# Optimization experiments

Hardware: AMD Instinct MI355X
Metric: run time of the kernel (lower is better)

## Reference

```python
import jax, jax.numpy as jnp
import numpy as np


def _norm(H, add):
    # Faithful port of GTN.norm: transpose, zero diagonal (optionally add self-loop),
    # row-degree inverse scaling, transpose back.
    Ht = H.T
    n = Ht.shape[0]
    eye = jnp.eye(n, dtype=H.dtype)
    Ht = Ht * (1.0 - eye) + (eye if add else 0.0)
    deg = jnp.sum(Ht, axis=1)
    dinv = jnp.where(deg == 0, 0.0, 1.0 / deg)
    return (dinv[:, None] * Ht).T


def _lstm(x, h0, c0, wih, whh, bih, bhh):
    # x: [B, S, D]; single-layer batch_first LSTM, PyTorch gate order (i, f, g, o).
    def step(carry, xt):
        h, c = carry
        gates = xt @ wih.T + h @ whh.T + bih + bhh
        i, f, g, o = jnp.split(gates, 4, axis=-1)
        i = jax.nn.sigmoid(i); f = jax.nn.sigmoid(f)
        g = jnp.tanh(g); o = jax.nn.sigmoid(o)
        c = f * c + i * g
        h = o * jnp.tanh(c)
        return (h, c), h
    (_, _), ys = jax.lax.scan(step, (h0, c0), jnp.transpose(x, (1, 0, 2)))
    return jnp.transpose(ys, (1, 0, 2))  # [B, S, U]


def _forward(A, X, seq_len, seqs, h0, c0, w1a, w1b, w2,
             gcn_w, lin1_w, lin1_b, lstm_wih, lstm_whh, lstm_bih, lstm_bhh, out_w):
    N = A.shape[0]
    B, S, _ = seqs.shape
    A4 = jnp.transpose(A, (2, 0, 1))  # [E, N, N]

    def gtconv(w):  # w: [C, E], softmax over edge-type channels
        return jnp.einsum('enm,ce->cnm', A4, jax.nn.softmax(w, axis=1))

    # layer 0 (first=True): H = conv1(A) @ conv2(A)
    H = jnp.matmul(gtconv(w1a), gtconv(w1b))  # [C, N, N]
    # layer 1: normalize per channel, then H = H_ @ conv1(A)
    Hn = jax.vmap(lambda h: _norm(h, False))(H)
    H = jnp.matmul(Hn, gtconv(w2))

    # gcn_conv per channel: relu(norm(H_c, add=True).T @ (X @ W)), concat over channels
    Hg = jax.vmap(lambda h: _norm(h, True))(H)  # [C, N, N]
    Xw = X @ gcn_w                              # [N, w_out]
    Xc = jax.nn.relu(jnp.einsum('cnm,nw->cmw', Hg, Xw))  # [C, N, w_out]
    X_ = jnp.transpose(Xc, (1, 0, 2)).reshape(N, -1) @ lin1_w.T + lin1_b  # [N, w_out]

    # ragged basket max-pool: masked segment-max over multi-hot baskets
    mask = seqs != 0                                           # [B, S, I]
    pooled = jnp.max(jnp.where(mask[:, :, :, None], X_[None, None], -jnp.inf), axis=2)
    basket_seqs = jnp.where(mask.any(axis=2)[..., None], pooled, 0.0)  # [B, S, w_out]

    lstm_out = _lstm(basket_seqs, h0[0], c0[0], lstm_wih, lstm_whh, lstm_bih, lstm_bhh)
    idx = jnp.clip(seq_len - 1, 0, S - 1)
    actual = lstm_out[jnp.arange(B), idx]      # [B, U]
    return jax.nn.sigmoid(actual @ out_w.T)    # [B, nb_items]


def setup_inputs() -> dict:
    N, E, C, WIN, WOUT, B, S, U = 2048, 4, 2, 64, 64, 16, 20, 256
    I = N  # nb_items
    key = jax.random.key(0)
    ks = jax.random.split(key, 16)
    A = jax.random.uniform(ks[0], (N, N, E), dtype=jnp.float32)
    X = jax.random.normal(ks[1], (N, WIN), dtype=jnp.float32)
    seq_len = jax.random.randint(ks[2], (B,), 1, S + 1)
    # sparse multi-hot baskets (~20 items per basket)
    seqs = (jax.random.uniform(ks[3], (B, S, I)) < 0.01).astype(jnp.int32)
    h0 = jnp.zeros((1, B, U), dtype=jnp.float32)
    c0 = jnp.zeros((1, B, U), dtype=jnp.float32)
    w1a = 0.1 * jax.random.normal(ks[4], (C, E), dtype=jnp.float32)
    w1b = 0.1 * jax.random.normal(ks[5], (C, E), dtype=jnp.float32)
    w2 = 0.1 * jax.random.normal(ks[6], (C, E), dtype=jnp.float32)
    gcn_w = jax.random.normal(ks[7], (WIN, WOUT), dtype=jnp.float32) / np.sqrt(WIN)
    lin1_w = 0.05 * jax.random.normal(ks[8], (WOUT, C * WOUT), dtype=jnp.float32)
    lin1_b = jnp.zeros((WOUT,), dtype=jnp.float32)
    lstm_wih = 0.05 * jax.random.normal(ks[9], (4 * U, WOUT), dtype=jnp.float32)
    lstm_whh = 0.05 * jax.random.normal(ks[10], (4 * U, U), dtype=jnp.float32)
    lstm_bih = jnp.zeros((4 * U,), dtype=jnp.float32)
    lstm_bhh = jnp.zeros((4 * U,), dtype=jnp.float32)
    out_w = 0.05 * jax.random.normal(ks[11], (I, U), dtype=jnp.float32)
    return {"A": A, "X": X, "seq_len": seq_len, "seqs": seqs, "h0": h0, "c0": c0,
            "w1a": w1a, "w1b": w1b, "w2": w2, "gcn_w": gcn_w,
            "lin1_w": lin1_w, "lin1_b": lin1_b, "lstm_wih": lstm_wih,
            "lstm_whh": lstm_whh, "lstm_bih": lstm_bih, "lstm_bhh": lstm_bhh,
            "out_w": out_w}


def reference(A, X, seq_len, seqs, h0, c0, w1a, w1b, w2, gcn_w, lin1_w, lin1_b,
              lstm_wih, lstm_whh, lstm_bih, lstm_bhh, out_w):
    return _forward(A, X, seq_len, seqs, h0, c0, w1a, w1b, w2, gcn_w,
                    lin1_w, lin1_b, lstm_wih, lstm_whh, lstm_bih, lstm_bhh, out_w)
```

## Files before the change

### kernel.cpp

```cpp
#include <hip/hip_runtime.h>
#include <hip/hip_fp16.h>
#include <math.h>

#define NN_ 2048
#define EE_ 4
#define CC_ 2
#define BB_ 16
#define SS_ 20
#define UU_ 256

#define LREGB 80
#define LLDSB 48

typedef __attribute__((ext_vector_type(8))) short short8;
typedef __attribute__((ext_vector_type(4))) float f32x4;
typedef _Float16 half2v __attribute__((ext_vector_type(2)));

__device__ __forceinline__ unsigned short f2bf(float x){
    union { float f; unsigned int u; } v; v.f = x;
    unsigned int u = v.u;
    unsigned int r = u + 0x7FFFu + ((u >> 16) & 1u);
    return (unsigned short)(r >> 16);
}
__device__ __forceinline__ float bf2f(unsigned short s){
    union { unsigned int u; float f; } v; v.u = ((unsigned int)s) << 16; return v.f;
}

__device__ __forceinline__ half2v u2h2(unsigned int u){
    union { unsigned int u; half2v h; } c; c.u = u; return c.h;
}

__device__ __forceinline__ float dot2f(unsigned int w, unsigned int h, float acc){
#if __has_builtin(__builtin_amdgcn_fdot2)
    return __builtin_amdgcn_fdot2(u2h2(w), u2h2(h), acc, false);
#else
    float w0 = __half2float(__ushort_as_half((unsigned short)(w & 0xffffu)));
    float w1 = __half2float(__ushort_as_half((unsigned short)(w >> 16)));
    float h0f = __half2float(__ushort_as_half((unsigned short)(h & 0xffffu)));
    float h1f = __half2float(__ushort_as_half((unsigned short)(h >> 16)));
    return fmaf(w1, h1f, fmaf(w0, h0f, acc));
#endif
}

__device__ __forceinline__ float sigf(float x){
    x = fminf(fmaxf(x, -30.f), 30.f);
    float e = __builtin_amdgcn_exp2f(-1.442695041f * x);
    return __builtin_amdgcn_rcpf(1.f + e);
}
__device__ __forceinline__ float tanhf_(float x){
    x = fminf(fmaxf(x, -15.f), 15.f);
    float e = __builtin_amdgcn_exp2f(2.885390082f * x);
    return (e - 1.f) * __builtin_amdgcn_rcpf(e + 1.f);
}

typedef const __attribute__((address_space(1))) unsigned int* gas_ptr;
typedef __attribute__((address_space(3))) unsigned int* las_ptr;
__device__ __forceinline__ void gl_lds16(const void* g, void* l){
    __builtin_amdgcn_global_load_lds((gas_ptr)g, (las_ptr)l, 16, 0, 0);
}

__global__ void k_softmax(const float* __restrict__ w1a, const float* __restrict__ w1b,
                          const float* __restrict__ w2, float* __restrict__ sm){
    int t = threadIdx.x;
    if (t < 6){
        int widx = t >> 1, c = t & 1;
        const float* w = (widx==0)? w1a : ((widx==1)? w1b : w2);
        float v[EE_]; float m = -1e30f;
        for (int e=0;e<EE_;e++){ v[e]=w[c*EE_+e]; m=fmaxf(m,v[e]); }
        float s=0.f;
        for (int e=0;e<EE_;e++){ v[e]=expf(v[e]-m); s+=v[e]; }
        for (int e=0;e<EE_;e++) sm[widx*8 + c*4 + e] = v[e]/s;
    }
}

__global__ __launch_bounds__(256) void k_conv_bf16(const float4* __restrict__ A4,
        const float* __restrict__ sm, unsigned short* __restrict__ convA,
        unsigned short* __restrict__ convBT, unsigned short* __restrict__ convCT){
    __shared__ float4 tile[32][33];
    int bx = blockIdx.x*32, by = blockIdx.y*32;
    int tx = threadIdx.x & 31, ty = threadIdx.x >> 5;
    #pragma unroll
    for (int i=0;i<32;i+=8){
        int n = by+ty+i, m = bx+tx;
        float4 a = A4[(size_t)n*NN_ + m];
        tile[ty+i][tx] = a;
        #pragma unroll
        for (int cc=0;cc<CC_;cc++){
            const float* s = sm + cc*4;
            convA[(size_t)cc*NN_*NN_ + (size_t)n*NN_ + m] =
                f2bf(a.x*s[0]+a.y*s[1]+a.z*s[2]+a.w*s[3]);
        }
    }
    __syncthreads();
    #pragma unroll
    for (int i=0;i<32;i+=8){
        int x = bx+ty+i, y = by+tx;
        float4 a = tile[tx][ty+i];
        #pragma unroll
        for (int cc=0;cc<CC_;cc++){
            const float* s1 = sm + 8 + cc*4;
            const float* s2 = sm + 16 + cc*4;
            convBT[(size_t)cc*NN_*NN_ + (size_t)x*NN_ + y] =
                f2bf(a.x*s1[0]+a.y*s1[1]+a.z*s1[2]+a.w*s1[3]);
            convCT[(size_t)cc*NN_*NN_ + (size_t)x*NN_ + y] =
                f2bf(a.x*s2[0]+a.y*s2[1]+a.z*s2[2]+a.w*s2[3]);
        }
    }
}

__global__ __launch_bounds__(256) void k_mfma_gemm(const unsigned short* __restrict__ Abase,
        const unsigned short* __restrict__ Bbase, unsigned short* __restrict__ Cbase,
        float* __restrict__ colbase){
    const int c = blockIdx.z;
    const unsigned short* Ag = Abase + (size_t)c*NN_*NN_;
    const unsigned short* Bg = Bbase + (size_t)c*NN_*NN_;
    unsigned short* Cg = Cbase + (size_t)c*NN_*NN_;
    float* colacc = colbase + c*NN_;

    __shared__ __align__(16) unsigned short As[128*32];
    __shared__ __align__(16) unsigned short Bs[128*32];

    const int t = threadIdx.x;
    const int wave = t >> 6, lane = t & 63;
    const int m0 = blockIdx.y*128, n0 = blockIdx.x*128;
    const int wm = wave >> 1, wn = wave & 1;

    f32x4 acc[4][4];
    const f32x4 z = {0.f,0.f,0.f,0.f};
    #pragma unroll
    for (int i=0;i<4;i++)
        #pragma unroll
        for (int j=0;j<4;j++) acc[i][j] = z;

    const int srow = wave*32 + (lane>>2);
    const int scol = (lane&3)*8;
    const unsigned short* agp0 = Ag + (size_t)(m0+srow)*NN_ + scol;
    const unsigned short* agp1 = agp0 + (size_t)16*NN_;
    const unsigned short* bgp0 = Bg + (size_t)(n0+srow)*NN_ + scol;
    const unsigned short* bgp1 = bgp0 + (size_t)16*NN_;
    unsigned short* alp0 = &As[wave*1024];
    unsigned short* alp1 = &As[wave*1024 + 512];
    unsigned short* blp0 = &Bs[wave*1024];
    unsigned short* blp1 = &Bs[wave*1024 + 512];

    const int fr = lane & 15;
    const int fk = (lane >> 4) * 8;

    for (int k0=0; k0<NN_; k0+=32){
        gl_lds16(agp0, alp0);
        gl_lds16(agp1, alp1);
        gl_lds16(bgp0, blp0);
        gl_lds16(bgp1, blp1);
        agp0 += 32; agp1 += 32; bgp0 += 32; bgp1 += 32;
        __syncthreads();
        short8 af[4], bf[4];
        #pragma unroll
        for (int i=0;i<4;i++){
            af[i] = *(const short8*)&As[(wm*64 + i*16 + fr)*32 + fk];
            bf[i] = *(const short8*)&Bs[(wn*64 + i*16 + fr)*32 + fk];
        }
        #pragma unroll
        for (int i=0;i<4;i++)
            #pragma unroll
            for (int j=0;j<4;j++)
                acc[i][j] = __builtin_amdgcn_mfma_f32_16x16x32_bf16(af[i], bf[j], acc[i][j], 0, 0, 0);
        __syncthreads();
    }

    #pragma unroll
    for (int j=0;j<4;j++){
        int col = n0 + wn*64 + j*16 + (lane & 15);
        float cs = 0.f;
        #pragma unroll
        for (int i=0;i<4;i++){
            int row = m0 + wm*64 + i*16 + (lane>>4)*4;
            #pragma unroll
            for (int r=0;r<4;r++){
                Cg[(size_t)(row+r)*NN_ + col] = f2bf(acc[i][j][r]);
                cs += acc[i][j][r];
            }
        }
        atomicAdd(&colacc[col], cs);
    }
}

template<bool ADD>
__global__ void k_dinv(float* acc, const unsigned short* __restrict__ H){
    int id = blockIdx.x*256 + threadIdx.x;
    int c = id / NN_, m = id % NN_;
    float diag = bf2f(H[(size_t)c*NN_*NN_ + (size_t)m*NN_ + m]);
    float s = acc[id] - diag + (ADD ? 1.f : 0.f);
    acc[id] = (s==0.f) ? 0.f : 1.f/s;
}

__global__ __launch_bounds__(256) void k_hn(const unsigned short* __restrict__ H1,
        const float* __restrict__ dinv, unsigned short* __restrict__ Hn){
    int id = blockIdx.x*256 + threadIdx.x;
    int c = id >> 20;
    int rem = id & ((NN_*NN_/4)-1);
    int m = rem >> 9;
    int k4 = (rem & (NN_/4 - 1)) * 4;
    ushort4 h = *(const ushort4*)&H1[(size_t)c*NN_*NN_ + (size_t)m*NN_ + k4];
    float4 d = *(const float4*)&dinv[c*NN_ + k4];
    ushort4 o;
    o.x = f2bf((m==k4  ) ? 0.f : bf2f(h.x)*d.x);
    o.y = f2bf((m==k4+1) ? 0.f : bf2f(h.y)*d.y);
    o.z = f2bf((m==k4+2) ? 0.f : bf2f(h.z)*d.z);
    o.w = f2bf((m==k4+3) ? 0.f : bf2f(h.w)*d.w);
    *(ushort4*)&Hn[(size_t)c*NN_*NN_ + (size_t)m*NN_ + k4] = o;
}

__global__ __launch_bounds__(256) void k_xw(const float* __restrict__ X, const float* __restrict__ W,
                                            float* __restrict__ Xw){
    __shared__ float Ws[64*64];
    int t = threadIdx.x;
    for (int i=t;i<4096;i+=256) Ws[i]=W[i];
    __syncthreads();
    int id = blockIdx.x*256 + t;
    int n = id >> 6, w = id & 63;
    float s = 0.f;
    #pragma unroll 8
    for (int j=0;j<64;j++) s = fmaf(X[n*64+j], Ws[j*64+w], s);
    Xw[id] = s;
}

__global__ __launch_bounds__(256) void k_gcn(const unsigned short* __restrict__ H2,
                                             const float* __restrict__ Xw, float* __restrict__ Y){
    int c = blockIdx.z;
    int m0 = blockIdx.y*64;
    int n0 = blockIdx.x*256;
    const unsigned short* Hc = H2 + (size_t)c*NN_*NN_;
    __shared__ float Hs[16][68];
    __shared__ float Xs[16][68];
    int t = threadIdx.x;
    int tm = t>>4, tn = t&15;
    float acc[4][4] = {};
    for (int nb=n0; nb<n0+256; nb+=16){
        int row = t>>4, c4 = (t&15)<<2;
        ushort4 h4 = *(const ushort4*)&Hc[(size_t)(nb+row)*NN_ + m0 + c4];
        Hs[row][c4+0]=bf2f(h4.x); Hs[row][c4+1]=bf2f(h4.y);
        Hs[row][c4+2]=bf2f(h4.z); Hs[row][c4+3]=bf2f(h4.w);
        *(float4*)&Xs[row][c4] = *(const float4*)&Xw[(nb+row)*64 + c4];
        __syncthreads();
        #pragma unroll
        for (int k=0;k<16;k++){
            float4 av = *(const float4*)&Hs[k][tm*4];
            float4 bv = *(const float4*)&Xs[k][tn*4];
            float a[4] = {av.x,av.y,av.z,av.w};
            float b[4] = {bv.x,bv.y,bv.z,bv.w};
            #pragma unroll
            for (int i=0;i<4;i++)
                #pragma unroll
                for (int j=0;j<4;j++)
                    acc[i][j] = fmaf(a[i], b[j], acc[i][j]);
        }
        __syncthreads();
    }
    #pragma unroll
    for (int i=0;i<4;i++)
        #pragma unroll
        for (int j=0;j<4;j++)
            atomicAdd(&Y[((size_t)c*NN_ + m0+tm*4+i)*64 + tn*4+j], acc[i][j]);
}

__global__ void k_gcn_epi(const float* __restrict__ Y, const unsigned short* __restrict__ H2,
                          const float* __restrict__ Xw, const float* __restrict__ dinv2,
                          float* __restrict__ Xcat){
    int id = blockIdx.x*256 + threadIdx.x;
    int c = id >> 17;
    int rem = id & 131071;
    int m = rem >> 6, w = rem & 63;
    float diag = bf2f(H2[(size_t)c*NN_*NN_ + (size_t)m*NN_ + m]);
    float xwv = Xw[m*64+w];
    float v = dinv2[c*NN_+m] * (Y[id] - diag*xwv + xwv);
    Xcat[m*128 + c*64 + w] = fmaxf(v, 0.f);
}

__global__ __launch_bounds__(256) void k_lin1(const float* __restrict__ Xcat, const float* __restrict__ W,
                                              const float* __restrict__ b, float* __restrict__ Xf){
    __shared__ float WT[128*64];
    __shared__ float bs[64];
    int t = threadIdx.x;
    for (int i=t;i<8192;i+=256){ int o = i>>7, j = i&127; WT[j*64+o] = W[i]; }
    if (t<64) bs[t]=b[t];
    __syncthreads();
    int id = blockIdx.x*256 + t;
    int m = id>>6, o = id&63;
    float s = bs[o];
    #pragma unroll 8
    for (int j=0;j<128;j++) s = fmaf(Xcat[m*128+j], WT[j*64+o], s);
    Xf[id] = s;
}

__global__ __launch_bounds__(256) void k_pool(const int* __restrict__ seqs, const float* __restrict__ Xf,
                                              float* __restrict__ bask){
    int bs_id = blockIdx.x;
    __shared__ int idxbuf[NN_];
    __shared__ int cnt;
    __shared__ float red[4][64];
    int t = threadIdx.x;
    if (t==0) cnt=0;
    __syncthreads();
    const int* row = seqs + (size_t)bs_id*NN_;
    for (int i=t;i<NN_;i+=256){
        if (row[i] != 0){ int p = atomicAdd(&cnt,1); idxbuf[p]=i; }
    }
    __syncthreads();
    int nc = cnt;
    int g = t>>6, w = t&63;
    float mx = -INFINITY;
    for (int p=g;p<nc;p+=4) mx = fmaxf(mx, Xf[idxbuf[p]*64 + w]);
    red[g][w]=mx;
    __syncthreads();
    if (t<64){
        float m = fmaxf(fmaxf(red[0][t],red[1][t]),fmaxf(red[2][t],red[3][t]));
        bask[bs_id*64+t] = (nc>0)? m : 0.f;
    }
}

__global__ void k_transpose(const float* __restrict__ src, float* __restrict__ dst, int R, int Cc){
    __shared__ float tile[32][33];
    int bx = blockIdx.x*32, by = blockIdx.y*32;
    int tx = threadIdx.x, ty = threadIdx.y;
    #pragma unroll
    for (int i=0;i<32;i+=8) tile[ty+i][tx] = src[(size_t)(by+ty+i)*Cc + bx+tx];
    __syncthreads();
    #pragma unroll
    for (int i=0;i<32;i+=8) dst[(size_t)(bx+ty+i)*R + by+tx] = tile[tx][ty+i];
}

__global__ __launch_bounds__(256) void k_packw2(const float* __restrict__ whh, unsigned int* __restrict__ W2k){
    int id = blockIdx.x*256 + threadIdx.x;
    int rem = id >> 7;
    int jp  = id & 127;
    float2 v = *(const float2*)&whh[(size_t)rem*256 + 2*jp];
    unsigned int lo = __half_as_ushort(__float2half(v.x));
    unsigned int hi = __half_as_ushort(__float2half(v.y));
    W2k[id] = lo | (hi << 16);
}

__global__ __launch_bounds__(256) void k_gih(const float* __restrict__ bask, const float* __restrict__ wihT,
                                             const float* __restrict__ bih, const float* __restrict__ bhh,
                                             float* __restrict__ G){
    int id = blockIdx.x*256 + threadIdx.x;
    int r = id >> 10, o = id & 1023;
    float s = bih[o] + bhh[o];
    #pragma unroll 8
    for (int j=0;j<64;j++) s = fmaf(bask[r*64+j], wihT[j*1024+o], s);
    G[id] = s;
}

__global__ __launch_bounds__(512, 2) void k_lstm4(const unsigned int* __restrict__ W2k,
        const float* __restrict__ G, const float* __restrict__ h0, const float* __restrict__ c0,
        const int* __restrict__ seqlen, float* __restrict__ actual){
    const int b = blockIdx.x;
    const int t = threadIdx.x;
    const int u = t & 255;
    const int half_ = t >> 8;
    const int g0 = 2*half_;
    const int g1 = g0 + 1;

    __shared__ unsigned int Wl[LLDSB][2][256];
    __shared__ unsigned int hpk[128];
    __shared__ float xg[256], xo[256];

    for (int k=0;k<LLDSB;k++){
        int idx = k*512 + t;
        int jj = idx >> 9, rem = idx & 511;
        int hf = rem >> 8, uu = rem & 255;
        ((unsigned int*)Wl)[idx] = W2k[(size_t)((2*hf+1)*256 + uu)*128 + LREGB + jj];
    }
    unsigned int wA[128], wB[LREGB];
    const unsigned int* pA = W2k + (size_t)(g0*256 + u)*128;
    const unsigned int* pB = W2k + (size_t)(g1*256 + u)*128;
    #pragma unroll
    for (int jp=0;jp<128;jp++) wA[jp] = pA[jp];
    #pragma unroll
    for (int jp=0;jp<LREGB;jp++) wB[jp] = pB[jp];

    float cv = 0.f;
    if (half_==0){
        cv = c0[b*256+u];
        ((__half*)hpk)[u] = __float2half(h0[b*256+u]);
    }
    int sl = seqlen[b]-1;
    int idx_b = sl<0?0:(sl>SS_-1?SS_-1:sl);
    __syncthreads();

    const float* gbase = G + (size_t)b*SS_*1024;
    for (int s=0;s<SS_;s++){
        float gA = gbase[s*1024 + g0*256 + u];
        float gB = gbase[s*1024 + g1*256 + u];
        float aA[4] = {0.f,0.f,0.f,0.f};
        float aB[4] = {0.f,0.f,0.f,0.f};
        #pragma unroll
        for (int jp=0;jp<LREGB;jp++){
            unsigned int hp = hpk[jp];
            aA[jp&3] = dot2f(wA[jp], hp, aA[jp&3]);
            aB[jp&3] = dot2f(wB[jp], hp, aB[jp&3]);
        }
        #pragma unroll
        for (int jp=LREGB;jp<128;jp++){
            unsigned int hp = hpk[jp];
            aA[jp&3] = dot2f(wA[jp], hp, aA[jp&3]);
            aB[jp&3] = dot2f(Wl[jp-LREGB][half_][u], hp, aB[jp&3]);
        }
        float accA = (aA[0]+aA[1]) + (aA[2]+aA[3]) + gA;
        float accB = (aB[0]+aB[1]) + (aB[2]+aB[3]) + gB;
        float iv = 0.f, fv = 0.f;
        if (half_){
            xg[u] = tanhf_(accA);
            xo[u] = sigf(accB);
        } else {
            iv = sigf(accA);
            fv = sigf(accB);
        }
        __syncthreads();
        if (!half_){
            cv = fv*cv + iv*xg[u];
            float hv = xo[u]*tanhf_(cv);
            if (s==idx_b) actual[b*256+u] = hv;
            ((__half*)hpk)[u] = __float2half(hv);
        }
        __syncthreads();
    }
}

__global__ __launch_bounds__(256) void k_final(const float* __restrict__ actual, const float* __restrict__ owT,
                                               float* __restrict__ out){
    __shared__ float as_[256];
    int t = threadIdx.x;
    int b = blockIdx.x >> 3;
    int i0 = (blockIdx.x & 7) * 256;
    as_[t] = actual[b*256+t];
    __syncthreads();
    int i = i0 + t;
    float s = 0.f;
    #pragma unroll 8
    for (int u=0;u<256;u++) s = fmaf(as_[u], owT[u*2048 + i], s);
    out[b*2048 + i] = 1.f/(1.f+expf(-s));
}

extern "C" void kernel_launch(void* const* d_in, const int* in_sizes, int n_in,
                              void* d_out, int out_size, void* d_ws, size_t ws_size,
                              hipStream_t stream){
    const float* A     = (const float*)d_in[0];
    const float* X     = (const float*)d_in[1];
    const int*   seqln = (const int*)  d_in[2];
    const int*   seqs  = (const int*)  d_in[3];
    const float* h0    = (const float*)d_in[4];
    const float* c0    = (const float*)d_in[5];
    const float* w1a   = (const float*)d_in[6];
    const float* w1b   = (const float*)d_in[7];
    const float* w2    = (const float*)d_in[8];
    const float* gcn_w = (const float*)d_in[9];
    const float* lin1w = (const float*)d_in[10];
    const float* lin1b = (const float*)d_in[11];
    const float* wih   = (const float*)d_in[12];
    const float* whh   = (const float*)d_in[13];
    const float* bih   = (const float*)d_in[14];
    const float* bhh   = (const float*)d_in[15];
    const float* out_w = (const float*)d_in[16];
    float* out = (float*)d_out;

    char* ws = (char*)d_ws;
    size_t off = 0;
    auto alloc = [&](size_t bytes)->char*{
        char* p = ws + off; off += (bytes + 255) & ~(size_t)255; return p;
    };
    float* sm     = (float*)alloc(24*4);
    float* dinv1  = (float*)alloc(CC_*NN_*4);
    float* dinv2  = (float*)alloc(CC_*NN_*4);
    float* Xw     = (float*)alloc((size_t)NN_*64*4);
    float* Xcat   = (float*)alloc((size_t)NN_*128*4);
    float* Xf     = (float*)alloc((size_t)NN_*64*4);
    float* Ybuf   = (float*)alloc((size_t)CC_*NN_*64*4);
    float* bask   = (float*)alloc((size_t)BB_*SS_*64*4);
    float* Gih    = (float*)alloc((size_t)BB_*SS_*1024*4);
    unsigned int* W2k = (unsigned int*)alloc((size_t)1024*128*4);
    float* wihT   = (float*)alloc((size_t)64*1024*4);
    float* owT    = (float*)alloc((size_t)256*2048*4);
    float* actual = (float*)alloc((size_t)BB_*UU_*4);
    unsigned short* convA  = (unsigned short*)alloc((size_t)CC_*NN_*NN_*2);
    unsigned short* convBT = (unsigned short*)alloc((size_t)CC_*NN_*NN_*2);
    unsigned short* convCT = (unsigned short*)alloc((size_t)CC_*NN_*NN_*2);
    unsigned short* HnB    = (unsigned short*)alloc((size_t)CC_*NN_*NN_*2);
    unsigned short* H1b    = (unsigned short*)alloc((size_t)CC_*NN_*NN_*2);
    unsigned short* H2b    = convA;

    hipMemsetAsync(dinv1, 0, CC_*NN_*4, stream);
    hipMemsetAsync(dinv2, 0, CC_*NN_*4, stream);
    hipMemsetAsync(Ybuf,  0, (size_t)CC_*NN_*64*4, stream);

    k_softmax<<<1,64,0,stream>>>(w1a,w1b,w2,sm);
    k_conv_bf16<<<dim3(64,64),256,0,stream>>>((const float4*)A, sm, convA, convBT, convCT);
    k_mfma_gemm<<<dim3(16,16,2),256,0,stream>>>(convA, convBT, H1b, dinv1);
    k_dinv<false><<<CC_*NN_/256,256,0,stream>>>(dinv1, H1b);
    k_hn<<<CC_*NN_*NN_/4/256,256,0,stream>>>(H1b, dinv1, HnB);
    k_mfma_gemm<<<dim3(16,16,2),256,0,stream>>>(HnB, convCT, H2b, dinv2);
    k_dinv<true><<<CC_*NN_/256,256,0,stream>>>(dinv2, H2b);
    k_xw<<<NN_*64/256,256,0,stream>>>(X, gcn_w, Xw);
    k_gcn<<<dim3(8,32,2),256,0,stream>>>(H2b, Xw, Ybuf);
    k_gcn_epi<<<CC_*NN_*64/256,256,0,stream>>>(Ybuf, H2b, Xw, dinv2, Xcat);
    k_lin1<<<NN_*64/256,256,0,stream>>>(Xcat, lin1w, lin1b, Xf);
    k_pool<<<BB_*SS_,256,0,stream>>>(seqs, Xf, bask);
    k_packw2<<<1024*128/256,256,0,stream>>>(whh, W2k);
    k_transpose<<<dim3(64/32, 1024/32),dim3(32,8),0,stream>>>(wih,  wihT, 1024, 64);
    k_transpose<<<dim3(256/32,2048/32),dim3(32,8),0,stream>>>(out_w, owT, 2048, 256);
    k_gih<<<BB_*SS_*1024/256,256,0,stream>>>(bask, wihT, bih, bhh, Gih);
    k_lstm4<<<BB_,512,0,stream>>>(W2k, Gih, h0, c0, seqln, actual);
    k_final<<<BB_*2048/256,256,0,stream>>>(actual, owT, out);
}
```

Baseline: 463.6 us.

## Deepen GEMM K-tile with XOR-swizzled LDS, remap blocks, split column sums

The bf16 MFMA GEMM now stages 64-wide K tiles per barrier pair instead of 32, using an XOR swizzle on the LDS chunk index to avoid bank conflicts. Blocks are launched as a 1D grid remapped so consecutive blocks spread across XCDs. The fused column-sum atomics are moved out of the GEMM epilogue into a separate colsum kernel that reads the bf16 result, and the softmax kernel is folded into the conversion kernel. Fewer barriers and conflict-free LDS reads should raise MFMA throughput, at the cost of an extra pass over the H matrices and column sums now taken from rounded bf16 values.

```diff
diff --git a/kernel.cpp b/kernel.cpp
--- a/kernel.cpp
+++ b/kernel.cpp
@@ -59,23 +59,22 @@
     __builtin_amdgcn_global_load_lds((gas_ptr)g, (las_ptr)l, 16, 0, 0);
 }
 
-__global__ void k_softmax(const float* __restrict__ w1a, const float* __restrict__ w1b,
-                          const float* __restrict__ w2, float* __restrict__ sm){
-    int t = threadIdx.x;
-    if (t < 6){
-        int widx = t >> 1, c = t & 1;
-        const float* w = (widx==0)? w1a : ((widx==1)? w1b : w2);
-        float v[EE_]; float m = -1e30f;
-        for (int e=0;e<EE_;e++){ v[e]=w[c*EE_+e]; m=fmaxf(m,v[e]); }
-        float s=0.f;
-        for (int e=0;e<EE_;e++){ v[e]=expf(v[e]-m); s+=v[e]; }
-        for (int e=0;e<EE_;e++) sm[widx*8 + c*4 + e] = v[e]/s;
-    }
+__device__ __forceinline__ void sm4(const float* __restrict__ w, int c, float* o){
+    float v0=w[c*4], v1=w[c*4+1], v2=w[c*4+2], v3=w[c*4+3];
+    float m = fmaxf(fmaxf(v0,v1), fmaxf(v2,v3));
+    float e0=expf(v0-m), e1=expf(v1-m), e2=expf(v2-m), e3=expf(v3-m);
+    float r = 1.f/(e0+e1+e2+e3);
+    o[0]=e0*r; o[1]=e1*r; o[2]=e2*r; o[3]=e3*r;
 }
 
 __global__ __launch_bounds__(256) void k_conv_bf16(const float4* __restrict__ A4,
-        const float* __restrict__ sm, unsigned short* __restrict__ convA,
-        unsigned short* __restrict__ convBT, unsigned short* __restrict__ convCT){
+        const float* __restrict__ w1a, const float* __restrict__ w1b, const float* __restrict__ w2,
+        unsigned short* __restrict__ convA, unsigned short* __restrict__ convBT,
+        unsigned short* __restrict__ convCT){
+    float smA[2][4], smB[2][4], smC[2][4];
+    #pragma unroll
+    for (int cc=0;cc<2;cc++){ sm4(w1a,cc,smA[cc]); sm4(w1b,cc,smB[cc]); sm4(w2,cc,smC[cc]); }
+
     __shared__ float4 tile[32][33];
     int bx = blockIdx.x*32, by = blockIdx.y*32;
     int tx = threadIdx.x & 31, ty = threadIdx.x >> 5;
@@ -86,7 +85,7 @@
         tile[ty+i][tx] = a;
         #pragma unroll
         for (int cc=0;cc<CC_;cc++){
-            const float* s = sm + cc*4;
+            const float* s = smA[cc];
             convA[(size_t)cc*NN_*NN_ + (size_t)n*NN_ + m] =
                 f2bf(a.x*s[0]+a.y*s[1]+a.z*s[2]+a.w*s[3]);
         }
@@ -98,8 +97,8 @@
         float4 a = tile[tx][ty+i];
         #pragma unroll
         for (int cc=0;cc<CC_;cc++){
-            const float* s1 = sm + 8 + cc*4;
-            const float* s2 = sm + 16 + cc*4;
+            const float* s1 = smB[cc];
+            const float* s2 = smC[cc];
             convBT[(size_t)cc*NN_*NN_ + (size_t)x*NN_ + y] =
                 f2bf(a.x*s1[0]+a.y*s1[1]+a.z*s1[2]+a.w*s1[3]);
             convCT[(size_t)cc*NN_*NN_ + (size_t)x*NN_ + y] =
@@ -109,20 +108,22 @@
 }
 
 __global__ __launch_bounds__(256) void k_mfma_gemm(const unsigned short* __restrict__ Abase,
-        const unsigned short* __restrict__ Bbase, unsigned short* __restrict__ Cbase,
-        float* __restrict__ colbase){
-    const int c = blockIdx.z;
+        const unsigned short* __restrict__ Bbase, unsigned short* __restrict__ Cbase){
+    const int bid = blockIdx.x;
+    const int nid = (bid & 7) * 64 + (bid >> 3);
+    const int n0 = (nid & 15) * 128;
+    const int m0 = ((nid >> 4) & 15) * 128;
+    const int c  = nid >> 8;
+
     const unsigned short* Ag = Abase + (size_t)c*NN_*NN_;
     const unsigned short* Bg = Bbase + (size_t)c*NN_*NN_;
     unsigned short* Cg = Cbase + (size_t)c*NN_*NN_;
-    float* colacc = colbase + c*NN_;
-
-    __shared__ __align__(16) unsigned short As[128*32];
-    __shared__ __align__(16) unsigned short Bs[128*32];
+
+    __shared__ __align__(16) unsigned short As[128*64];
+    __shared__ __align__(16) unsigned short Bs[128*64];
 
     const int t = threadIdx.x;
     const int wave = t >> 6, lane = t & 63;
-    const int m0 = blockIdx.y*128, n0 = blockIdx.x*128;
     const int wm = wave >> 1, wn = wave & 1;
 
     f32x4 acc[4][4];
@@ -132,56 +133,71 @@
         #pragma unroll
         for (int j=0;j<4;j++) acc[i][j] = z;
 
-    const int srow = wave*32 + (lane>>2);
-    const int scol = (lane&3)*8;
-    const unsigned short* agp0 = Ag + (size_t)(m0+srow)*NN_ + scol;
-    const unsigned short* agp1 = agp0 + (size_t)16*NN_;
-    const unsigned short* bgp0 = Bg + (size_t)(n0+srow)*NN_ + scol;
-    const unsigned short* bgp1 = bgp0 + (size_t)16*NN_;
-    unsigned short* alp0 = &As[wave*1024];
-    unsigned short* alp1 = &As[wave*1024 + 512];
-    unsigned short* blp0 = &Bs[wave*1024];
-    unsigned short* blp1 = &Bs[wave*1024 + 512];
+    const int lrow   = lane >> 3;
+    const int lchunk = lane & 7;
+    const int gchunk = lchunk ^ lrow;
+    const unsigned short* agp = Ag + (size_t)(m0 + wave*32 + lrow)*NN_ + gchunk*8;
+    const unsigned short* bgp = Bg + (size_t)(n0 + wave*32 + lrow)*NN_ + gchunk*8;
+    unsigned short* alp = &As[wave*32*64];
+    unsigned short* blp = &Bs[wave*32*64];
 
     const int fr = lane & 15;
-    const int fk = (lane >> 4) * 8;
-
-    for (int k0=0; k0<NN_; k0+=32){
-        gl_lds16(agp0, alp0);
-        gl_lds16(agp1, alp1);
-        gl_lds16(bgp0, blp0);
-        gl_lds16(bgp1, blp1);
-        agp0 += 32; agp1 += 32; bgp0 += 32; bgp1 += 32;
+    const int hi = lane >> 4;
+    const int sw = fr & 7;
+
+    for (int k0=0; k0<NN_; k0+=64){
+        #pragma unroll
+        for (int k=0;k<4;k++){
+            gl_lds16(agp + (size_t)k*8*NN_ + k0, alp + k*512);
+            gl_lds16(bgp + (size_t)k*8*NN_ + k0, blp + k*512);
+        }
         __syncthreads();
-        short8 af[4], bf[4];
+        short8 af[2][4], bf[2][4];
         #pragma unroll
         for (int i=0;i<4;i++){
-            af[i] = *(const short8*)&As[(wm*64 + i*16 + fr)*32 + fk];
-            bf[i] = *(const short8*)&Bs[(wn*64 + i*16 + fr)*32 + fk];
-        }
-        #pragma unroll
-        for (int i=0;i<4;i++)
+            int rowA = (wm*64 + i*16 + fr)*64;
+            int rowB = (wn*64 + i*16 + fr)*64;
+            af[0][i] = *(const short8*)&As[rowA + ((hi    ) ^ sw)*8];
+            af[1][i] = *(const short8*)&As[rowA + ((hi + 4) ^ sw)*8];
+            bf[0][i] = *(const short8*)&Bs[rowB + ((hi    ) ^ sw)*8];
+            bf[1][i] = *(const short8*)&Bs[rowB + ((hi + 4) ^ sw)*8];
+        }
+        #pragma unroll
+        for (int kk=0;kk<2;kk++)
             #pragma unroll
-            for (int j=0;j<4;j++)
-                acc[i][j] = __builtin_amdgcn_mfma_f32_16x16x32_bf16(af[i], bf[j], acc[i][j], 0, 0, 0);
+            for (int i=0;i<4;i++)
+                #pragma unroll
+                for (int j=0;j<4;j++)
+                    acc[i][j] = __builtin_amdgcn_mfma_f32_16x16x32_bf16(af[kk][i], bf[kk][j], acc[i][j], 0, 0, 0);
         __syncthreads();
     }
 
     #pragma unroll
-    for (int j=0;j<4;j++){
-        int col = n0 + wn*64 + j*16 + (lane & 15);
-        float cs = 0.f;
-        #pragma unroll
-        for (int i=0;i<4;i++){
-            int row = m0 + wm*64 + i*16 + (lane>>4)*4;
+    for (int i=0;i<4;i++){
+        int row = m0 + wm*64 + i*16 + hi*4;
+        #pragma unroll
+        for (int j=0;j<4;j++){
+            int col = n0 + wn*64 + j*16 + fr;
             #pragma unroll
-            for (int r=0;r<4;r++){
+            for (int r=0;r<4;r++)
                 Cg[(size_t)(row+r)*NN_ + col] = f2bf(acc[i][j][r]);
-                cs += acc[i][j][r];
-            }
-        }
-        atomicAdd(&colacc[col], cs);
-    }
+        }
+    }
+}
+
+__global__ __launch_bounds__(256) void k_colsum_bf(const unsigned short* __restrict__ H,
+                                                   float* __restrict__ acc){
+    int c = blockIdx.z;
+    int mp = blockIdx.x*256 + threadIdx.x;
+    int nbeg = blockIdx.y*128;
+    const unsigned short* Hc = H + (size_t)c*NN_*NN_;
+    float s0 = 0.f, s1 = 0.f;
+    for (int n=nbeg;n<nbeg+128;n++){
+        ushort2 u = *(const ushort2*)&Hc[(size_t)n*NN_ + 2*mp];
+        s0 += bf2f(u.x); s1 += bf2f(u.y);
+    }
+    atomicAdd(&acc[c*NN_ + 2*mp],     s0);
+    atomicAdd(&acc[c*NN_ + 2*mp + 1], s1);
 }
 
 template<bool ADD>
@@ -468,7 +484,6 @@
     auto alloc = [&](size_t bytes)->char*{
         char* p = ws + off; off += (bytes + 255) & ~(size_t)255; return p;
     };
-    float* sm     = (float*)alloc(24*4);
     float* dinv1  = (float*)alloc(CC_*NN_*4);
     float* dinv2  = (float*)alloc(CC_*NN_*4);
     float* Xw     = (float*)alloc((size_t)NN_*64*4);
@@ -492,12 +507,13 @@
     hipMemsetAsync(dinv2, 0, CC_*NN_*4, stream);
     hipMemsetAsync(Ybuf,  0, (size_t)CC_*NN_*64*4, stream);
 
-    k_softmax<<<1,64,0,stream>>>(w1a,w1b,w2,sm);
-    k_conv_bf16<<<dim3(64,64),256,0,stream>>>((const float4*)A, sm, convA, convBT, convCT);
-    k_mfma_gemm<<<dim3(16,16,2),256,0,stream>>>(convA, convBT, H1b, dinv1);
+    k_conv_bf16<<<dim3(64,64),256,0,stream>>>((const float4*)A, w1a, w1b, w2, convA, convBT, convCT);
+    k_mfma_gemm<<<512,256,0,stream>>>(convA, convBT, H1b);
+    k_colsum_bf<<<dim3(4,16,2),256,0,stream>>>(H1b, dinv1);
     k_dinv<false><<<CC_*NN_/256,256,0,stream>>>(dinv1, H1b);
     k_hn<<<CC_*NN_*NN_/4/256,256,0,stream>>>(H1b, dinv1, HnB);
-    k_mfma_gemm<<<dim3(16,16,2),256,0,stream>>>(HnB, convCT, H2b, dinv2);
+    k_mfma_gemm<<<512,256,0,stream>>>(HnB, convCT, H2b);
+    k_colsum_bf<<<dim3(4,16,2),256,0,stream>>>(H2b, dinv2);
     k_dinv<true><<<CC_*NN_/256,256,0,stream>>>(dinv2, H2b);
     k_xw<<<NN_*64/256,256,0,stream>>>(X, gcn_w, Xw);
     k_gcn<<<dim3(8,32,2),256,0,stream>>>(H2b, Xw, Ybuf);
```

After: 405.5 us. -12.5%, faster.
